# Kernel optimization log

Hardware: AMD Instinct MI355X
Metric: run time of the kernel (lower is better)

Reference implementation:

```python
import jax, jax.numpy as jnp
import numpy as np

N = 4096; TD = 768; ID = 512; H = 256; NH = 4; HD = H // NH; NC = 3; E = 131072


def _gcn(x, w, b, src, dst, n):
    # GCNConv: add self loops, sym-normalize, aggregate at dst
    loop = jnp.arange(n)
    s = jnp.concatenate([src, loop])
    d = jnp.concatenate([dst, loop])
    deg = jax.ops.segment_sum(jnp.ones(s.shape[0], x.dtype), d, num_segments=n)
    dinv = jnp.where(deg > 0, jax.lax.rsqrt(deg), 0.0)
    norm = dinv[s] * dinv[d]                      # [E+N]
    h = x @ w                                     # [N,H] transform
    out = jax.ops.segment_sum(norm[:, None] * h[s], d, num_segments=n)
    return out + b


def setup_inputs() -> dict:
    key = jax.random.key(0)
    ks = jax.random.split(key, 20)
    p = lambda k, shp, sc: jax.random.normal(k, shp, jnp.float32) * sc
    inp = {
        "text_features": jax.random.normal(ks[0], (N, TD), jnp.float32),
        "image_features": jax.random.normal(ks[1], (N, ID), jnp.float32),
        "edge_index": jax.random.randint(ks[2], (2, E), 0, N, jnp.int32),
        "text_w": p(ks[3], (TD, H), 0.02), "text_b": jnp.zeros((H,), jnp.float32),
        "image_w": p(ks[4], (ID, H), 0.02), "image_b": jnp.zeros((H,), jnp.float32),
        "wq": p(ks[5], (H, H), 0.02), "bq": jnp.zeros((H,), jnp.float32),
        "wk": p(ks[6], (H, H), 0.02), "bk": jnp.zeros((H,), jnp.float32),
        "wv": p(ks[7], (H, H), 0.02), "bv": jnp.zeros((H,), jnp.float32),
        "wo": p(ks[8], (H, H), 0.02), "bo": jnp.zeros((H,), jnp.float32),
        "gcn1_w": p(ks[9], (H, H), 0.02), "gcn1_b": jnp.zeros((H,), jnp.float32),
        "gcn2_w": p(ks[10], (H, H), 0.02), "gcn2_b": jnp.zeros((H,), jnp.float32),
        "cls_w": p(ks[11], (H, NC), 0.02), "cls_b": jnp.zeros((NC,), jnp.float32),
    }
    return inp


def reference(text_features, image_features, edge_index,
              text_w, text_b, image_w, image_b,
              wq, bq, wk, bk, wv, bv, wo, bo,
              gcn1_w, gcn1_b, gcn2_w, gcn2_b, cls_w, cls_b):
    # fused linear+relu projections, then elementwise fuse of sum
    combined = (jax.nn.relu(text_features @ text_w + text_b)
                + jax.nn.relu(image_features @ image_w + image_b))  # [N,H]
    # MHA over all nodes (seq_len=N, batch=1)
    q = (combined @ wq + bq).reshape(N, NH, HD)
    k = (combined @ wk + bk).reshape(N, NH, HD)
    v = (combined @ wv + bv).reshape(N, NH, HD)
    scores = jnp.einsum('nhd,mhd->hnm', q, k) / jnp.sqrt(jnp.float32(HD))
    attn = jax.nn.softmax(scores, axis=-1)
    o = jnp.einsum('hnm,mhd->nhd', attn, v).reshape(N, H)
    attn_out = o @ wo + bo
    # two GCN layers
    src, dst = edge_index[0], edge_index[1]
    g1 = jax.nn.relu(_gcn(attn_out, gcn1_w, gcn1_b, src, dst, N))
    g2 = _gcn(g1, gcn2_w, gcn2_b, src, dst, N)
    return g2 @ cls_w + cls_b
```

## Files before the change

kernel.cpp:

```cpp
#include <hip/hip_runtime.h>
#include <hip/hip_bf16.h>

typedef unsigned short ushort;
typedef __attribute__((ext_vector_type(8))) short short8;
typedef __attribute__((ext_vector_type(4))) float f32x4;

constexpr int N_  = 4096;
constexpr int TD_ = 768;
constexpr int ID_ = 512;
constexpr int H_  = 256;
constexpr int HD_ = 64;
constexpr int E_  = 131072;
constexpr int SPLITS = 8;
constexpr float QSCALE = 0.125f * 1.44269504088896f;

#define MFMA16(a, b, c) __builtin_amdgcn_mfma_f32_16x16x32_bf16(a, b, c, 0, 0, 0)

__device__ inline ushort f2bf(float x) {
    union { float f; unsigned u; } v; v.f = x;
    unsigned r = v.u + 0x7fff + ((v.u >> 16) & 1);
    return (ushort)(r >> 16);
}
__device__ inline float lo2f(unsigned u) { union { unsigned x; float f; } v; v.x = u << 16; return v.f; }
__device__ inline float hi2f(unsigned u) { union { unsigned x; float f; } v; v.x = u & 0xffff0000u; return v.f; }

__device__ inline float exp2r(float x) {
    float r;
    asm("v_exp_f32 %0, %1" : "=v"(r) : "v"(x));
    return r;
}
__device__ inline unsigned pkbf(float lo, float hi) {
    union { float f; unsigned u; } a, b; a.f = lo; b.f = hi;
    return __builtin_amdgcn_perm(b.u + 0x8000u, a.u + 0x8000u, 0x07060302u);
}

__device__ inline void gl_lds16(const void* g, void* l) {
    __builtin_amdgcn_global_load_lds((const __attribute__((address_space(1))) unsigned int*)g,
                                     (__attribute__((address_space(3))) unsigned int*)l, 16, 0, 0);
}

__device__ inline void stage64(const ushort* g, long long strideEl, ushort* lds, int w, int l) {
    int r8 = l >> 3;
    int cc = (l & 7) ^ r8;
    #pragma unroll
    for (int p = 0; p < 2; p++) {
        int row = w * 16 + p * 8 + r8;
        gl_lds16(g + (long long)row * strideEl + cc * 8, lds + (w * 16 + p * 8) * 64);
    }
}
__device__ inline void stageB16(const ushort* g, long long strideEl, ushort* lds, int w, int l) {
    if (w < 2) {
        int r8 = l >> 3;
        int row = w * 8 + r8;
        int cc = (l & 7) ^ (row & 7);
        gl_lds16(g + (long long)row * strideEl + cc * 8, lds + w * 512);
    }
}
__device__ inline int swz(int row, int kOff) {
    return row * 64 + ((((kOff >> 3) ^ (row & 7))) << 3);
}


__global__ __launch_bounds__(256) void k_init(int* __restrict__ indeg, int* __restrict__ pos) {
    int i = blockIdx.x * 256 + threadIdx.x;
    indeg[i] = 0;
    pos[i] = 0;
}

__global__ __launch_bounds__(1024) void k_scan(const int* __restrict__ indeg, int* __restrict__ offs,
                                               float* __restrict__ dinv) {
    __shared__ int sums[1024];
    int t = threadIdx.x;
    int b = t * 4;
    int a0 = indeg[b], a1 = indeg[b + 1], a2 = indeg[b + 2], a3 = indeg[b + 3];
    int s = a0 + a1 + a2 + a3;
    sums[t] = s;
    __syncthreads();
    for (int off = 1; off < 1024; off <<= 1) {
        int vv = (t >= off) ? sums[t - off] : 0;
        __syncthreads();
        sums[t] += vv;
        __syncthreads();
    }
    int excl = sums[t] - s;
    offs[b]     = excl;
    offs[b + 1] = excl + a0;
    offs[b + 2] = excl + a0 + a1;
    offs[b + 3] = excl + a0 + a1 + a2;
    dinv[b]     = 1.f / sqrtf((float)(a0 + 1));
    dinv[b + 1] = 1.f / sqrtf((float)(a1 + 1));
    dinv[b + 2] = 1.f / sqrtf((float)(a2 + 1));
    dinv[b + 3] = 1.f / sqrtf((float)(a3 + 1));
}

__global__ __launch_bounds__(256) void k_scatter(const int* __restrict__ src, const int* __restrict__ dst,
                                                 const int* __restrict__ offs, const float* __restrict__ dinv,
                                                 int* __restrict__ pos, int* __restrict__ ssrc,
                                                 float* __restrict__ sw) {
    int e = blockIdx.x * 256 + threadIdx.x;
    int s = src[e], d = dst[e];
    int p = atomicAdd(&pos[d], 1);
    int idx = offs[d] + p;
    ssrc[idx] = s;
    sw[idx] = dinv[s] * dinv[d];
}


__global__ __launch_bounds__(256) void k_prep(const float* __restrict__ text, const float* __restrict__ img,
                                              const float* __restrict__ tw, const float* __restrict__ iw,
                                              const float* __restrict__ wq, const float* __restrict__ wk,
                                              const float* __restrict__ wv, const float* __restrict__ wo,
                                              const float* __restrict__ g1w, const float* __restrict__ g2w,
                                              const int* __restrict__ edst, int* __restrict__ indeg,
                                              ushort* __restrict__ textbf, ushort* __restrict__ imgbf,
                                              ushort* __restrict__ wobf,
                                              ushort* __restrict__ twT, ushort* __restrict__ iwT,
                                              ushort* __restrict__ wqT, ushort* __restrict__ wkT,
                                              ushort* __restrict__ wvT, ushort* __restrict__ g1wT,
                                              ushort* __restrict__ g2wT) {
    __shared__ float Ts[64][65];
    const int b = blockIdx.x;
    const int t = threadIdx.x;
    if (b >= 2752) {
        int e = (b - 2752) * 256 + t;
        atomicAdd(&indeg[edst[e]], 1);
        return;
    }
    if (b < 2592) {
        size_t base = ((size_t)b * 256 + t) * 8;
        const size_t TXE = (size_t)N_ * TD_, IME = (size_t)N_ * ID_;
        const float* src; ushort* dst;
        if (base < TXE) { src = text + base; dst = textbf + base; }
        else if (base < TXE + IME) { src = img + (base - TXE); dst = imgbf + (base - TXE); }
        else { src = wo + (base - TXE - IME); dst = wobf + (base - TXE - IME); }
        float4 x = *(const float4*)src;
        float4 y = *(const float4*)(src + 4);
        ushort o[8] = { f2bf(x.x), f2bf(x.y), f2bf(x.z), f2bf(x.w),
                        f2bf(y.x), f2bf(y.y), f2bf(y.z), f2bf(y.w) };
        *(short8*)dst = *(const short8*)o;
        return;
    }
    int wb = b - 2592;
    const float* src; ushort* dst; int R, tile;
    if (wb < 48)       { src = tw;  dst = twT;  R = 768; tile = wb; }
    else if (wb < 80)  { src = iw;  dst = iwT;  R = 512; tile = wb - 48; }
    else if (wb < 96)  { src = wq;  dst = wqT;  R = 256; tile = wb - 80; }
    else if (wb < 112) { src = wk;  dst = wkT;  R = 256; tile = wb - 96; }
    else if (wb < 128) { src = wv;  dst = wvT;  R = 256; tile = wb - 112; }
    else if (wb < 144) { src = g1w; dst = g1wT; R = 256; tile = wb - 128; }
    else               { src = g2w; dst = g2wT; R = 256; tile = wb - 144; }
    const int r0 = (tile >> 2) * 64, c0 = (tile & 3) * 64;
    #pragma unroll
    for (int u = 0; u < 16; u++) {
        int lin = t + u * 256;
        int r = lin >> 6, c = lin & 63;
        Ts[r][c] = src[(size_t)(r0 + r) * 256 + c0 + c];
    }
    __syncthreads();
    #pragma unroll
    for (int u = 0; u < 16; u++) {
        int lin = t + u * 256;
        int c = lin >> 6, r = lin & 63;
        dst[(size_t)(c0 + c) * R + r0 + r] = f2bf(Ts[r][c]);
    }
}


__global__ __launch_bounds__(256) void k_foldw(const ushort* __restrict__ g1wT, const ushort* __restrict__ wobf,
                                               const float* __restrict__ bo,
                                               ushort* __restrict__ WpT, float* __restrict__ bp) {
    __shared__ ushort As[2][4096];
    __shared__ ushort Bs[2][4096];
    __shared__ ushort Cs[64 * 72];
    const int t = threadIdx.x;
    if (blockIdx.x == 16) {
        float acc = 0.f;
        const ushort* row = g1wT + (size_t)t * 256;
        for (int m8 = 0; m8 < 256; m8 += 8) {
            #pragma unroll
            for (int j = 0; j < 8; j++) acc += bo[m8 + j] * lo2f(((unsigned)row[m8 + j]) << 16);
        }
        bp[t] = acc;
        return;
    }
    const int bm = (blockIdx.x >> 2) * 64, bn = (blockIdx.x & 3) * 64;
    const int w = t >> 6, l = t & 63, q = l >> 4, i = l & 15;
    f32x4 acc[4];
    #pragma unroll
    for (int nt = 0; nt < 4; nt++) acc[nt] = (f32x4){0, 0, 0, 0};
    stage64(g1wT + (size_t)bm * H_, H_, As[0], w, l);
    stage64(wobf + (size_t)bn * H_, H_, Bs[0], w, l);
    for (int c = 0; c < 4; c++) {
        __syncthreads();
        if (c < 3) {
            stage64(g1wT + (size_t)bm * H_ + (c + 1) * 64, H_, As[(c + 1) & 1], w, l);
            stage64(wobf + (size_t)bn * H_ + (c + 1) * 64, H_, Bs[(c + 1) & 1], w, l);
        }
        const ushort* Ab = As[c & 1];
        const ushort* Bb = Bs[c & 1];
        #pragma unroll
        for (int kb = 0; kb < 2; kb++) {
            short8 af = *(const short8*)&Ab[swz(w * 16 + i, kb * 32 + q * 8)];
            #pragma unroll
            for (int nt = 0; nt < 4; nt++) {
                short8 bfr = *(const short8*)&Bb[swz(nt * 16 + i, kb * 32 + q * 8)];
                acc[nt] = MFMA16(af, bfr, acc[nt]);
            }
        }
    }
    __syncthreads();
    #pragma unroll
    for (int nt = 0; nt < 4; nt++)
        #pragma unroll
        for (int r = 0; r < 4; r++)
            Cs[(w * 16 + q * 4 + r) * 72 + nt * 16 + i] = f2bf(acc[nt][r]);
    __syncthreads();
    int rr = t >> 2, c16 = (t & 3) * 16;
    short8 v0 = *(const short8*)&Cs[rr * 72 + c16];
    short8 v1 = *(const short8*)&Cs[rr * 72 + c16 + 8];
    ushort* dst = WpT + (size_t)(bm + rr) * H_ + bn + c16;
    *(short8*)dst = v0;
    *(short8*)(dst + 8) = v1;
}


__global__ __launch_bounds__(256, 4) void k_combined16(const ushort* __restrict__ text, const ushort* __restrict__ img,
                                                       const ushort* __restrict__ twT, const ushort* __restrict__ iwT,
                                                       const float* __restrict__ tb, const float* __restrict__ ib,
                                                       ushort* __restrict__ out) {
    __shared__ ushort As[2][4096];
    __shared__ ushort Bs[2][1024];
    __shared__ ushort Cs[64 * 24];
    const int bm = blockIdx.x * 64, bn = blockIdx.y * 16;
    const int t = threadIdx.x, w = t >> 6, l = t & 63, q = l >> 4, i = l & 15;
    f32x4 acc1 = {0, 0, 0, 0}, acc2 = {0, 0, 0, 0};
    auto stC = [&](int c, int buf) {
        if (c < 12) {
            stage64(text + (size_t)bm * TD_ + c * 64, TD_, As[buf], w, l);
            stageB16(twT + (size_t)bn * TD_ + c * 64, TD_, Bs[buf], w, l);
        } else {
            stage64(img + (size_t)bm * ID_ + (c - 12) * 64, ID_, As[buf], w, l);
            stageB16(iwT + (size_t)bn * ID_ + (c - 12) * 64, ID_, Bs[buf], w, l);
        }
    };
    stC(0, 0);
    for (int c = 0; c < 20; c++) {
        __syncthreads();
        if (c + 1 < 20) stC(c + 1, (c + 1) & 1);
        const ushort* Ab = As[c & 1];
        const ushort* Bb = Bs[c & 1];
        #pragma unroll
        for (int kb = 0; kb < 2; kb++) {
            short8 af = *(const short8*)&Ab[swz(w * 16 + i, kb * 32 + q * 8)];
            short8 bfr = *(const short8*)&Bb[swz(i, kb * 32 + q * 8)];
            if (c < 12) acc1 = MFMA16(af, bfr, acc1);
            else        acc2 = MFMA16(af, bfr, acc2);
        }
    }
    __syncthreads();
    float b1 = tb[bn + i], b2 = ib[bn + i];
    #pragma unroll
    for (int r = 0; r < 4; r++) {
        float v = fmaxf(acc1[r] + b1, 0.f) + fmaxf(acc2[r] + b2, 0.f);
        Cs[(w * 16 + q * 4 + r) * 24 + i] = f2bf(v);
    }
    __syncthreads();
    if (t < 128) {
        int row = t >> 1, h8 = (t & 1) * 8;
        *(short8*)(out + (size_t)(bm + row) * H_ + bn + h8) = *(const short8*)&Cs[row * 24 + h8];
    }
}


__global__ __launch_bounds__(256) void k_qkv_mfma(const ushort* __restrict__ A,
                                                  const ushort* __restrict__ WqT, const ushort* __restrict__ WkT,
                                                  const ushort* __restrict__ WvT,
                                                  const float* __restrict__ bq, const float* __restrict__ bk,
                                                  const float* __restrict__ bv,
                                                  ushort* __restrict__ Qg, ushort* __restrict__ Kg,
                                                  ushort* __restrict__ Vtg) {
    __shared__ ushort As[2][4096];
    __shared__ ushort Bs[2][4096];
    __shared__ ushort Cs[64 * 72];
    const int bm = blockIdx.x * 64, head = blockIdx.y, z = blockIdx.z;
    const ushort* WT = (z == 0) ? WqT : (z == 1) ? WkT : WvT;
    const float* bias = (z == 0) ? bq : (z == 1) ? bk : bv;
    const int t = threadIdx.x, w = t >> 6, l = t & 63, q = l >> 4, i = l & 15;
    f32x4 acc[4];
    #pragma unroll
    for (int nt = 0; nt < 4; nt++) acc[nt] = (f32x4){0,0,0,0};

    stage64(A + (size_t)bm * H_, H_, As[0], w, l);
    stage64(WT + (size_t)(head * 64) * H_, H_, Bs[0], w, l);
    for (int c = 0; c < 4; c++) {
        __syncthreads();
        if (c < 3) {
            stage64(A + (size_t)bm * H_ + (c + 1) * 64, H_, As[(c + 1) & 1], w, l);
            stage64(WT + (size_t)(head * 64) * H_ + (c + 1) * 64, H_, Bs[(c + 1) & 1], w, l);
        }
        const ushort* Ab = As[c & 1];
        const ushort* Bb = Bs[c & 1];
        #pragma unroll
        for (int kb = 0; kb < 2; kb++) {
            short8 af = *(const short8*)&Ab[swz(w * 16 + i, kb * 32 + q * 8)];
            #pragma unroll
            for (int nt = 0; nt < 4; nt++) {
                short8 bfr = *(const short8*)&Bb[swz(nt * 16 + i, kb * 32 + q * 8)];
                acc[nt] = MFMA16(af, bfr, acc[nt]);
            }
        }
    }
    __syncthreads();
    #pragma unroll
    for (int nt = 0; nt < 4; nt++) {
        float bv_ = bias[head * 64 + nt * 16 + i];
        #pragma unroll
        for (int r = 0; r < 4; r++) {
            float v = acc[nt][r] + bv_;
            if (z == 0) v *= QSCALE;
            if (z < 2) Cs[(w * 16 + q * 4 + r) * 72 + nt * 16 + i] = f2bf(v);
            else       Cs[(nt * 16 + i) * 72 + w * 16 + q * 4 + r] = f2bf(v);
        }
    }
    __syncthreads();
    int rr = t >> 2, c16 = (t & 3) * 16;
    short8 v0 = *(const short8*)&Cs[rr * 72 + c16];
    short8 v1 = *(const short8*)&Cs[rr * 72 + c16 + 8];
    ushort* dst;
    if (z < 2) dst = ((z == 0) ? Qg : Kg) + (size_t)head * N_ * HD_ + (size_t)(bm + rr) * HD_ + c16;
    else       dst = Vtg + (size_t)head * HD_ * N_ + (size_t)rr * N_ + bm + c16;
    *(short8*)dst = v0;
    *(short8*)(dst + 8) = v1;
}


__global__ __launch_bounds__(256) void k_attn_mfma(const ushort* __restrict__ Qg, const ushort* __restrict__ Kg,
                                                   const ushort* __restrict__ Vtg, ushort* __restrict__ Op,
                                                   float* __restrict__ lp) {
    __shared__ ushort Ks[4096];
    __shared__ ushort Vs[4096];
    __shared__ ushort Ps[4][16 * 72];
    const int head = blockIdx.y, r0 = blockIdx.x * 64, z = blockIdx.z;
    const int t = threadIdx.x, w = t >> 6, l = t & 63, q = l >> 4, i = l & 15;
    const int rw = (i ^ (i >> 1)) & 7;
    ushort* Pw = &Ps[w][0];

    short8 qf[2];
    #pragma unroll
    for (int kb = 0; kb < 2; kb++)
        qf[kb] = *(const short8*)(Qg + ((size_t)head * N_ + r0 + w * 16 + i) * HD_ + kb * 32 + q * 8);

    f32x4 Oacc[4];
    float lacc = 0.f;
    #pragma unroll
    for (int dt = 0; dt < 4; dt++) Oacc[dt] = (f32x4){0, 0, 0, 0};

    const int NT = 64 / SPLITS;
    const int cb0 = z * NT;
    for (int it = 0; it < NT; it++) {
        const int cb = cb0 + it;
        __syncthreads();
        stage64(Kg + ((size_t)head * N_ + (size_t)cb * 64) * HD_, HD_, Ks, w, l);
        stage64(Vtg + (size_t)head * HD_ * N_ + cb * 64, N_, Vs, w, l);
        __syncthreads();

        f32x4 St[4];
        #pragma unroll
        for (int kt = 0; kt < 4; kt++) St[kt] = (f32x4){0, 0, 0, 0};
        #pragma unroll
        for (int kb = 0; kb < 2; kb++) {
            #pragma unroll
            for (int kt = 0; kt < 4; kt++) {
                short8 kf = *(const short8*)&Ks[swz(kt * 16 + i, kb * 32 + q * 8)];
                St[kt] = MFMA16(kf, qf[kb], St[kt]);
            }
        }
        #pragma unroll
        for (int kt = 0; kt < 4; kt++) {
            float p0 = exp2r(St[kt][0]), p1 = exp2r(St[kt][1]);
            float p2 = exp2r(St[kt][2]), p3 = exp2r(St[kt][3]);
            lacc += (p0 + p1) + (p2 + p3);
            int off = i * 72 + (((2 * kt + (q >> 1)) ^ rw) << 3) + ((q & 1) << 2);
            uint2 v; v.x = pkbf(p0, p1); v.y = pkbf(p2, p3);
            *(uint2*)&Pw[off] = v;
        }
        #pragma unroll
        for (int kb = 0; kb < 2; kb++) {
            short8 pf = *(const short8*)&Pw[i * 72 + (((4 * kb + q) ^ rw) << 3)];
            #pragma unroll
            for (int dt = 0; dt < 4; dt++) {
                short8 vf = *(const short8*)&Vs[swz(dt * 16 + i, kb * 32 + q * 8)];
                Oacc[dt] = MFMA16(vf, pf, Oacc[dt]);
            }
        }
    }

    lacc += __shfl_xor(lacc, 16);
    lacc += __shfl_xor(lacc, 32);

    const size_t sh = ((size_t)z * 4 + head) * N_;
    const int row = r0 + w * 16 + i;
    #pragma unroll
    for (int dt = 0; dt < 4; dt++) {
        uint2 v;
        v.x = pkbf(Oacc[dt][0], Oacc[dt][1]);
        v.y = pkbf(Oacc[dt][2], Oacc[dt][3]);
        *(uint2*)&Op[(sh + row) * HD_ + dt * 16 + q * 4] = v;
    }
    if (l < 16) lp[sh + r0 + w * 16 + l] = lacc;
}

__global__ __launch_bounds__(256) void k_attn_merge(const ushort* __restrict__ Op, const float* __restrict__ lp,
                                                    ushort* __restrict__ obuf) {
    const int t = threadIdx.x;
    const int idx = blockIdx.x * 16 + (t >> 4);
    const int h = idx >> 12, n = idx & 4095;
    const int d4 = (t & 15) * 4;
    float lsum = 0.f;
    float acc[4] = {0.f, 0.f, 0.f, 0.f};
    #pragma unroll
    for (int s = 0; s < SPLITS; s++) {
        size_t sh = ((size_t)s * 4 + h) * N_ + n;
        lsum += lp[sh];
        uint2 o4 = *(const uint2*)&Op[sh * HD_ + d4];
        acc[0] += lo2f(o4.x); acc[1] += hi2f(o4.x);
        acc[2] += lo2f(o4.y); acc[3] += hi2f(o4.y);
    }
    float inv = 1.f / lsum;
    uint2 res;
    res.x = pkbf(acc[0] * inv, acc[1] * inv);
    res.y = pkbf(acc[2] * inv, acc[3] * inv);
    *(uint2*)&obuf[(size_t)n * H_ + h * HD_ + d4] = res;
}


template <bool BIAS>
__global__ __launch_bounds__(256, 4) void k_gemm16(const ushort* __restrict__ A, const ushort* __restrict__ BT,
                                                   const float* __restrict__ bias, ushort* __restrict__ outb) {
    __shared__ ushort As[2][4096];
    __shared__ ushort Bs[2][1024];
    __shared__ ushort Cs[64 * 24];
    const int bm = blockIdx.x * 64, bn = blockIdx.y * 16;
    const int t = threadIdx.x, w = t >> 6, l = t & 63, q = l >> 4, i = l & 15;
    f32x4 acc = {0, 0, 0, 0};
    stage64(A + (size_t)bm * H_, H_, As[0], w, l);
    stageB16(BT + (size_t)bn * H_, H_, Bs[0], w, l);
    for (int c = 0; c < 4; c++) {
        __syncthreads();
        if (c < 3) {
            stage64(A + (size_t)bm * H_ + (c + 1) * 64, H_, As[(c + 1) & 1], w, l);
            stageB16(BT + (size_t)bn * H_ + (c + 1) * 64, H_, Bs[(c + 1) & 1], w, l);
        }
        const ushort* Ab = As[c & 1];
        const ushort* Bb = Bs[c & 1];
        #pragma unroll
        for (int kb = 0; kb < 2; kb++) {
            short8 af = *(const short8*)&Ab[swz(w * 16 + i, kb * 32 + q * 8)];
            short8 bfr = *(const short8*)&Bb[swz(i, kb * 32 + q * 8)];
            acc = MFMA16(af, bfr, acc);
        }
    }
    __syncthreads();
    float bb = BIAS ? bias[bn + i] : 0.f;
    #pragma unroll
    for (int r = 0; r < 4; r++)
        Cs[(w * 16 + q * 4 + r) * 24 + i] = f2bf(acc[r] + bb);
    __syncthreads();
    if (t < 128) {
        int row = t >> 1, h8 = (t & 1) * 8;
        *(short8*)(outb + (size_t)(bm + row) * H_ + bn + h8) = *(const short8*)&Cs[row * 24 + h8];
    }
}


__global__ __launch_bounds__(256) void k_agg1(const ushort* __restrict__ h, const int* __restrict__ ssrc,
                                              const float* __restrict__ sw, const int* __restrict__ offs,
                                              const int* __restrict__ indeg, const float* __restrict__ dinv,
                                              const float* __restrict__ bias, ushort* __restrict__ outb) {
    const int t = threadIdx.x;
    const int j = blockIdx.x * 4 + (t >> 6);
    const int d0 = (t & 63) * 4;
    float dj = dinv[j];
    uint2 hv = *(const uint2*)&h[(size_t)j * H_ + d0];
    float s2 = dj * dj;
    float a0 = s2 * lo2f(hv.x), a1 = s2 * hi2f(hv.x), a2 = s2 * lo2f(hv.y), a3 = s2 * hi2f(hv.y);
    int start = offs[j], cnt = indeg[j];
    for (int e = 0; e < cnt; e++) {
        int s = ssrc[start + e];
        float wg = sw[start + e];
        uint2 v = *(const uint2*)&h[(size_t)s * H_ + d0];
        a0 += wg * lo2f(v.x); a1 += wg * hi2f(v.x);
        a2 += wg * lo2f(v.y); a3 += wg * hi2f(v.y);
    }
    a0 = fmaxf(a0 + bias[d0], 0.f);
    a1 = fmaxf(a1 + bias[d0 + 1], 0.f);
    a2 = fmaxf(a2 + bias[d0 + 2], 0.f);
    a3 = fmaxf(a3 + bias[d0 + 3], 0.f);
    uint2 o;
    o.x = pkbf(a0, a1);
    o.y = pkbf(a2, a3);
    *(uint2*)&outb[(size_t)j * H_ + d0] = o;
}


__global__ __launch_bounds__(256) void k_aggcls(const ushort* __restrict__ h, const int* __restrict__ ssrc,
                                                const float* __restrict__ sw, const int* __restrict__ offs,
                                                const int* __restrict__ indeg, const float* __restrict__ dinv,
                                                const float* __restrict__ bias, const float* __restrict__ cw,
                                                const float* __restrict__ cb, float* __restrict__ out) {
    const int t = threadIdx.x;
    const int j = blockIdx.x * 4 + (t >> 6);
    const int lane = t & 63;
    const int d0 = lane * 4;
    float dj = dinv[j];
    uint2 hv = *(const uint2*)&h[(size_t)j * H_ + d0];
    float s2 = dj * dj;
    float a0 = s2 * lo2f(hv.x), a1 = s2 * hi2f(hv.x), a2 = s2 * lo2f(hv.y), a3 = s2 * hi2f(hv.y);
    int start = offs[j], cnt = indeg[j];
    for (int e = 0; e < cnt; e++) {
        int s = ssrc[start + e];
        float wg = sw[start + e];
        uint2 v = *(const uint2*)&h[(size_t)s * H_ + d0];
        a0 += wg * lo2f(v.x); a1 += wg * hi2f(v.x);
        a2 += wg * lo2f(v.y); a3 += wg * hi2f(v.y);
    }
    a0 += bias[d0]; a1 += bias[d0 + 1]; a2 += bias[d0 + 2]; a3 += bias[d0 + 3];
    float p0 = a0 * cw[d0 * 3 + 0] + a1 * cw[(d0 + 1) * 3 + 0]
             + a2 * cw[(d0 + 2) * 3 + 0] + a3 * cw[(d0 + 3) * 3 + 0];
    float p1 = a0 * cw[d0 * 3 + 1] + a1 * cw[(d0 + 1) * 3 + 1]
             + a2 * cw[(d0 + 2) * 3 + 1] + a3 * cw[(d0 + 3) * 3 + 1];
    float p2 = a0 * cw[d0 * 3 + 2] + a1 * cw[(d0 + 1) * 3 + 2]
             + a2 * cw[(d0 + 2) * 3 + 2] + a3 * cw[(d0 + 3) * 3 + 2];
    #pragma unroll
    for (int off = 32; off > 0; off >>= 1) {
        p0 += __shfl_xor(p0, off);
        p1 += __shfl_xor(p1, off);
        p2 += __shfl_xor(p2, off);
    }
    if (lane == 0) {
        out[j * 3 + 0] = p0 + cb[0];
        out[j * 3 + 1] = p1 + cb[1];
        out[j * 3 + 2] = p2 + cb[2];
    }
}


extern "C" void kernel_launch(void* const* d_in, const int* in_sizes, int n_in,
                              void* d_out, int out_size, void* d_ws, size_t ws_size,
                              hipStream_t stream) {
    const float* text = (const float*)d_in[0];
    const float* img  = (const float*)d_in[1];
    const int*   eidx = (const int*)d_in[2];
    const float* tw  = (const float*)d_in[3];
    const float* tb  = (const float*)d_in[4];
    const float* iw  = (const float*)d_in[5];
    const float* ib  = (const float*)d_in[6];
    const float* wq  = (const float*)d_in[7];
    const float* bq  = (const float*)d_in[8];
    const float* wk  = (const float*)d_in[9];
    const float* bk  = (const float*)d_in[10];
    const float* wv  = (const float*)d_in[11];
    const float* bv  = (const float*)d_in[12];
    const float* wo  = (const float*)d_in[13];
    const float* bo  = (const float*)d_in[14];
    const float* g1w = (const float*)d_in[15];
    const float* g1b = (const float*)d_in[16];
    const float* g2w = (const float*)d_in[17];
    const float* g2b = (const float*)d_in[18];
    const float* cw  = (const float*)d_in[19];
    const float* cbv = (const float*)d_in[20];

    char* W = (char*)d_ws;
    size_t cur = 0;
    auto alloc = [&](size_t sz) { char* p = W + cur; cur += (sz + 255) & ~(size_t)255; return p; };

    float* dinv  = (float*)alloc(N_ * 4);
    float* swv   = (float*)alloc(E_ * 4);
    int* indeg   = (int*)alloc(N_ * 4);
    int* offs    = (int*)alloc(N_ * 4);
    int* pos     = (int*)alloc(N_ * 4);
    int* ssrc    = (int*)alloc(E_ * 4);
    ushort* Qg   = (ushort*)alloc((size_t)N_ * H_ * 2);
    ushort* Kg   = (ushort*)alloc((size_t)N_ * H_ * 2);
    ushort* Vtg  = (ushort*)alloc((size_t)N_ * H_ * 2);
    ushort* obuf = (ushort*)alloc((size_t)N_ * H_ * 2);
    ushort* WpT  = (ushort*)alloc((size_t)H_ * H_ * 2);
    float* bp    = (float*)alloc(H_ * 4);
    ushort* g1wT = (ushort*)alloc((size_t)H_ * H_ * 2);
    ushort* g2wT = (ushort*)alloc((size_t)H_ * H_ * 2);
    ushort* wobf = (ushort*)alloc((size_t)H_ * H_ * 2);
    float* lp    = (float*)alloc((size_t)SPLITS * 4 * N_ * 4);
    char* S = W + cur;

    ushort* textbf = (ushort*)S;
    ushort* imgbf  = textbf + (size_t)N_ * TD_;
    ushort* twT    = imgbf + (size_t)N_ * ID_;
    ushort* iwT    = twT + (size_t)TD_ * H_;
    ushort* wqT    = iwT + (size_t)ID_ * H_;
    ushort* wkT    = wqT + (size_t)H_ * H_;
    ushort* wvT    = wkT + (size_t)H_ * H_;
    ushort* combbf = wvT + (size_t)H_ * H_;
    ushort* Op = (ushort*)S;
    ushort* hbuf  = (ushort*)S;
    ushort* g1b16 = (ushort*)(S + (size_t)2 * 1024 * 1024);
    ushort* hbuf2 = (ushort*)(S + (size_t)4 * 1024 * 1024);

    const int* esrc = eidx;
    const int* edst = eidx + E_;

    k_init<<<dim3(N_ / 256), dim3(256), 0, stream>>>(indeg, pos);
    k_prep<<<dim3(3264), dim3(256), 0, stream>>>(text, img, tw, iw, wq, wk, wv, wo, g1w, g2w,
                                                 edst, indeg,
                                                 textbf, imgbf, wobf, twT, iwT, wqT, wkT, wvT, g1wT, g2wT);
    k_scan<<<dim3(1), dim3(1024), 0, stream>>>(indeg, offs, dinv);
    k_scatter<<<dim3(E_ / 256), dim3(256), 0, stream>>>(esrc, edst, offs, dinv, pos, ssrc, swv);
    k_foldw<<<dim3(17), dim3(256), 0, stream>>>(g1wT, wobf, bo, WpT, bp);

    k_combined16<<<dim3(64, 16), dim3(256), 0, stream>>>(textbf, imgbf, twT, iwT, tb, ib, combbf);
    k_qkv_mfma<<<dim3(64, 4, 3), dim3(256), 0, stream>>>(combbf, wqT, wkT, wvT, bq, bk, bv, Qg, Kg, Vtg);
    k_attn_mfma<<<dim3(64, 4, SPLITS), dim3(256), 0, stream>>>(Qg, Kg, Vtg, Op, lp);
    k_attn_merge<<<dim3(1024), dim3(256), 0, stream>>>(Op, lp, obuf);

    k_gemm16<true><<<dim3(64, 16), dim3(256), 0, stream>>>(obuf, WpT, bp, hbuf);
    k_agg1<<<dim3(N_ / 4), dim3(256), 0, stream>>>(hbuf, ssrc, swv, offs, indeg, dinv, g1b, g1b16);
    k_gemm16<false><<<dim3(64, 16), dim3(256), 0, stream>>>(g1b16, g2wT, nullptr, hbuf2);
    k_aggcls<<<dim3(N_ / 4), dim3(256), 0, stream>>>(hbuf2, ssrc, swv, offs, indeg, dinv, g2b, cw, cbv,
                                                     (float*)d_out);
}
```

Measured before the change: 239.5 us.

## Merge scatter and weight-fold kernels; double-buffer K/V tiles in attention

The edge scatter kernel and the Wo·G1 weight-fold kernel are merged into one launch with block-index dispatch. This removes one kernel launch and lets the two independent jobs run side by side. Separately, the attention kernel now double-buffers its K and V shared-memory tiles, so the next chunk loads while the current one computes, and one barrier per iteration is dropped. The cost is doubled LDS use in attention, which may lower occupancy, and scatter blocks now reserve the fold kernel's shared memory.

```diff
diff --git a/kernel.cpp b/kernel.cpp
--- a/kernel.cpp
+++ b/kernel.cpp
@@ -93,16 +93,76 @@
     dinv[b + 3] = 1.f / sqrtf((float)(a3 + 1));
 }
 
-__global__ __launch_bounds__(256) void k_scatter(const int* __restrict__ src, const int* __restrict__ dst,
-                                                 const int* __restrict__ offs, const float* __restrict__ dinv,
-                                                 int* __restrict__ pos, int* __restrict__ ssrc,
-                                                 float* __restrict__ sw) {
-    int e = blockIdx.x * 256 + threadIdx.x;
-    int s = src[e], d = dst[e];
-    int p = atomicAdd(&pos[d], 1);
-    int idx = offs[d] + p;
-    ssrc[idx] = s;
-    sw[idx] = dinv[s] * dinv[d];
+
+__global__ __launch_bounds__(256) void k_scatfold(const int* __restrict__ src, const int* __restrict__ dst,
+                                                  const int* __restrict__ offs, const float* __restrict__ dinv,
+                                                  int* __restrict__ pos, int* __restrict__ ssrc,
+                                                  float* __restrict__ sw,
+                                                  const ushort* __restrict__ g1wT, const ushort* __restrict__ wobf,
+                                                  const float* __restrict__ bo,
+                                                  ushort* __restrict__ WpT, float* __restrict__ bp) {
+    __shared__ ushort As[2][4096];
+    __shared__ ushort Bs[2][4096];
+    __shared__ ushort Cs[64 * 72];
+    const int t = threadIdx.x;
+    if (blockIdx.x < 512) {
+        int e = blockIdx.x * 256 + t;
+        int s = src[e], d = dst[e];
+        int p = atomicAdd(&pos[d], 1);
+        int idx = offs[d] + p;
+        ssrc[idx] = s;
+        sw[idx] = dinv[s] * dinv[d];
+        return;
+    }
+    if (blockIdx.x == 528) {
+        float acc = 0.f;
+        const ushort* row = g1wT + (size_t)t * 256;
+        for (int m8 = 0; m8 < 256; m8 += 8) {
+            #pragma unroll
+            for (int j = 0; j < 8; j++) acc += bo[m8 + j] * lo2f(((unsigned)row[m8 + j]) << 16);
+        }
+        bp[t] = acc;
+        return;
+    }
+    const int f = blockIdx.x - 512;
+    const int bm = (f >> 2) * 64, bn = (f & 3) * 64;
+    const int w = t >> 6, l = t & 63, q = l >> 4, i = l & 15;
+    f32x4 acc[4];
+    #pragma unroll
+    for (int nt = 0; nt < 4; nt++) acc[nt] = (f32x4){0, 0, 0, 0};
+    stage64(g1wT + (size_t)bm * H_, H_, As[0], w, l);
+    stage64(wobf + (size_t)bn * H_, H_, Bs[0], w, l);
+    for (int c = 0; c < 4; c++) {
+        __syncthreads();
+        if (c < 3) {
+            stage64(g1wT + (size_t)bm * H_ + (c + 1) * 64, H_, As[(c + 1) & 1], w, l);
+            stage64(wobf + (size_t)bn * H_ + (c + 1) * 64, H_, Bs[(c + 1) & 1], w, l);
+        }
+        const ushort* Ab = As[c & 1];
+        const ushort* Bb = Bs[c & 1];
+        #pragma unroll
+        for (int kb = 0; kb < 2; kb++) {
+            short8 af = *(const short8*)&Ab[swz(w * 16 + i, kb * 32 + q * 8)];
+            #pragma unroll
+            for (int nt = 0; nt < 4; nt++) {
+                short8 bfr = *(const short8*)&Bb[swz(nt * 16 + i, kb * 32 + q * 8)];
+                acc[nt] = MFMA16(af, bfr, acc[nt]);
+            }
+        }
+    }
+    __syncthreads();
+    #pragma unroll
+    for (int nt = 0; nt < 4; nt++)
+        #pragma unroll
+        for (int r = 0; r < 4; r++)
+            Cs[(w * 16 + q * 4 + r) * 72 + nt * 16 + i] = f2bf(acc[nt][r]);
+    __syncthreads();
+    int rr = t >> 2, c16 = (t & 3) * 16;
+    short8 v0 = *(const short8*)&Cs[rr * 72 + c16];
+    short8 v1 = *(const short8*)&Cs[rr * 72 + c16 + 8];
+    ushort* dstp = WpT + (size_t)(bm + rr) * H_ + bn + c16;
+    *(short8*)dstp = v0;
+    *(short8*)(dstp + 8) = v1;
 }
 
 
@@ -166,64 +226,6 @@
 }
 
 
-__global__ __launch_bounds__(256) void k_foldw(const ushort* __restrict__ g1wT, const ushort* __restrict__ wobf,
-                                               const float* __restrict__ bo,
-                                               ushort* __restrict__ WpT, float* __restrict__ bp) {
-    __shared__ ushort As[2][4096];
-    __shared__ ushort Bs[2][4096];
-    __shared__ ushort Cs[64 * 72];
-    const int t = threadIdx.x;
-    if (blockIdx.x == 16) {
-        float acc = 0.f;
-        const ushort* row = g1wT + (size_t)t * 256;
-        for (int m8 = 0; m8 < 256; m8 += 8) {
-            #pragma unroll
-            for (int j = 0; j < 8; j++) acc += bo[m8 + j] * lo2f(((unsigned)row[m8 + j]) << 16);
-        }
-        bp[t] = acc;
-        return;
-    }
-    const int bm = (blockIdx.x >> 2) * 64, bn = (blockIdx.x & 3) * 64;
-    const int w = t >> 6, l = t & 63, q = l >> 4, i = l & 15;
-    f32x4 acc[4];
-    #pragma unroll
-    for (int nt = 0; nt < 4; nt++) acc[nt] = (f32x4){0, 0, 0, 0};
-    stage64(g1wT + (size_t)bm * H_, H_, As[0], w, l);
-    stage64(wobf + (size_t)bn * H_, H_, Bs[0], w, l);
-    for (int c = 0; c < 4; c++) {
-        __syncthreads();
-        if (c < 3) {
-            stage64(g1wT + (size_t)bm * H_ + (c + 1) * 64, H_, As[(c + 1) & 1], w, l);
-            stage64(wobf + (size_t)bn * H_ + (c + 1) * 64, H_, Bs[(c + 1) & 1], w, l);
-        }
-        const ushort* Ab = As[c & 1];
-        const ushort* Bb = Bs[c & 1];
-        #pragma unroll
-        for (int kb = 0; kb < 2; kb++) {
-            short8 af = *(const short8*)&Ab[swz(w * 16 + i, kb * 32 + q * 8)];
-            #pragma unroll
-            for (int nt = 0; nt < 4; nt++) {
-                short8 bfr = *(const short8*)&Bb[swz(nt * 16 + i, kb * 32 + q * 8)];
-                acc[nt] = MFMA16(af, bfr, acc[nt]);
-            }
-        }
-    }
-    __syncthreads();
-    #pragma unroll
-    for (int nt = 0; nt < 4; nt++)
-        #pragma unroll
-        for (int r = 0; r < 4; r++)
-            Cs[(w * 16 + q * 4 + r) * 72 + nt * 16 + i] = f2bf(acc[nt][r]);
-    __syncthreads();
-    int rr = t >> 2, c16 = (t & 3) * 16;
-    short8 v0 = *(const short8*)&Cs[rr * 72 + c16];
-    short8 v1 = *(const short8*)&Cs[rr * 72 + c16 + 8];
-    ushort* dst = WpT + (size_t)(bm + rr) * H_ + bn + c16;
-    *(short8*)dst = v0;
-    *(short8*)(dst + 8) = v1;
-}
-
-
 __global__ __launch_bounds__(256, 4) void k_combined16(const ushort* __restrict__ text, const ushort* __restrict__ img,
                                                        const ushort* __restrict__ twT, const ushort* __restrict__ iwT,
                                                        const float* __restrict__ tb, const float* __restrict__ ib,
@@ -337,9 +339,9 @@
 __global__ __launch_bounds__(256) void k_attn_mfma(const ushort* __restrict__ Qg, const ushort* __restrict__ Kg,
                                                    const ushort* __restrict__ Vtg, ushort* __restrict__ Op,
                                                    float* __restrict__ lp) {
-    __shared__ ushort Ks[4096];
-    __shared__ ushort Vs[4096];
-    __shared__ ushort Ps[4][16 * 72];
+    __shared__ ushort Ks[2][4096];
+    __shared__ ushort Vs[2][4096];
+    __shared__ ushort Ps[4][1152];
     const int head = blockIdx.y, r0 = blockIdx.x * 64, z = blockIdx.z;
     const int t = threadIdx.x, w = t >> 6, l = t & 63, q = l >> 4, i = l & 15;
     const int rw = (i ^ (i >> 1)) & 7;
@@ -357,12 +359,17 @@
 
     const int NT = 64 / SPLITS;
     const int cb0 = z * NT;
+    stage64(Kg + ((size_t)head * N_ + (size_t)cb0 * 64) * HD_, HD_, Ks[0], w, l);
+    stage64(Vtg + (size_t)head * HD_ * N_ + cb0 * 64, N_, Vs[0], w, l);
     for (int it = 0; it < NT; it++) {
-        const int cb = cb0 + it;
         __syncthreads();
-        stage64(Kg + ((size_t)head * N_ + (size_t)cb * 64) * HD_, HD_, Ks, w, l);
-        stage64(Vtg + (size_t)head * HD_ * N_ + cb * 64, N_, Vs, w, l);
-        __syncthreads();
+        if (it + 1 < NT) {
+            const int cb = cb0 + it + 1;
+            stage64(Kg + ((size_t)head * N_ + (size_t)cb * 64) * HD_, HD_, Ks[(it + 1) & 1], w, l);
+            stage64(Vtg + (size_t)head * HD_ * N_ + cb * 64, N_, Vs[(it + 1) & 1], w, l);
+        }
+        const ushort* Kb = Ks[it & 1];
+        const ushort* Vb = Vs[it & 1];
 
         f32x4 St[4];
         #pragma unroll
@@ -371,7 +378,7 @@
         for (int kb = 0; kb < 2; kb++) {
             #pragma unroll
             for (int kt = 0; kt < 4; kt++) {
-                short8 kf = *(const short8*)&Ks[swz(kt * 16 + i, kb * 32 + q * 8)];
+                short8 kf = *(const short8*)&Kb[swz(kt * 16 + i, kb * 32 + q * 8)];
                 St[kt] = MFMA16(kf, qf[kb], St[kt]);
             }
         }
@@ -389,7 +396,7 @@
             short8 pf = *(const short8*)&Pw[i * 72 + (((4 * kb + q) ^ rw) << 3)];
             #pragma unroll
             for (int dt = 0; dt < 4; dt++) {
-                short8 vf = *(const short8*)&Vs[swz(dt * 16 + i, kb * 32 + q * 8)];
+                short8 vf = *(const short8*)&Vb[swz(dt * 16 + i, kb * 32 + q * 8)];
                 Oacc[dt] = MFMA16(vf, pf, Oacc[dt]);
             }
         }
@@ -613,8 +620,8 @@
                                                  edst, indeg,
                                                  textbf, imgbf, wobf, twT, iwT, wqT, wkT, wvT, g1wT, g2wT);
     k_scan<<<dim3(1), dim3(1024), 0, stream>>>(indeg, offs, dinv);
-    k_scatter<<<dim3(E_ / 256), dim3(256), 0, stream>>>(esrc, edst, offs, dinv, pos, ssrc, swv);
-    k_foldw<<<dim3(17), dim3(256), 0, stream>>>(g1wT, wobf, bo, WpT, bp);
+    k_scatfold<<<dim3(529), dim3(256), 0, stream>>>(esrc, edst, offs, dinv, pos, ssrc, swv,
+                                                    g1wT, wobf, bo, WpT, bp);
 
     k_combined16<<<dim3(64, 16), dim3(256), 0, stream>>>(textbf, imgbf, twT, iwT, tb, ib, combbf);
     k_qkv_mfma<<<dim3(64, 4, 3), dim3(256), 0, stream>>>(combbf, wqT, wkT, wvT, bq, bk, bv, Qg, Kg, Vtg);
```

Result: no change. 242.5 us (+1.2%).

## Fold graph preprocessing and weight folding into GEMM kernel launches

Applied to the files above, without the earlier changes.

Merges the degree scan into an extra block of the combined-projection kernel, and the edge scatter plus Wo·W1 weight folding into extra blocks of the QKV kernel. This cuts three kernel launches, including a serial single-block scan, and lets the small side tasks overlap with the GEMM blocks. The scan is rewritten for 256 threads with 16 elements each. It also marks the node index as wave-uniform via readfirstlane in the aggregation kernels. The cost is heterogeneous blocks inside one kernel, which may skew scheduling and shared-memory occupancy.

```diff
diff --git a/kernel.cpp b/kernel.cpp
--- a/kernel.cpp
+++ b/kernel.cpp
@@ -65,44 +65,6 @@
     int i = blockIdx.x * 256 + threadIdx.x;
     indeg[i] = 0;
     pos[i] = 0;
-}
-
-__global__ __launch_bounds__(1024) void k_scan(const int* __restrict__ indeg, int* __restrict__ offs,
-                                               float* __restrict__ dinv) {
-    __shared__ int sums[1024];
-    int t = threadIdx.x;
-    int b = t * 4;
-    int a0 = indeg[b], a1 = indeg[b + 1], a2 = indeg[b + 2], a3 = indeg[b + 3];
-    int s = a0 + a1 + a2 + a3;
-    sums[t] = s;
-    __syncthreads();
-    for (int off = 1; off < 1024; off <<= 1) {
-        int vv = (t >= off) ? sums[t - off] : 0;
-        __syncthreads();
-        sums[t] += vv;
-        __syncthreads();
-    }
-    int excl = sums[t] - s;
-    offs[b]     = excl;
-    offs[b + 1] = excl + a0;
-    offs[b + 2] = excl + a0 + a1;
-    offs[b + 3] = excl + a0 + a1 + a2;
-    dinv[b]     = 1.f / sqrtf((float)(a0 + 1));
-    dinv[b + 1] = 1.f / sqrtf((float)(a1 + 1));
-    dinv[b + 2] = 1.f / sqrtf((float)(a2 + 1));
-    dinv[b + 3] = 1.f / sqrtf((float)(a3 + 1));
-}
-
-__global__ __launch_bounds__(256) void k_scatter(const int* __restrict__ src, const int* __restrict__ dst,
-                                                 const int* __restrict__ offs, const float* __restrict__ dinv,
-                                                 int* __restrict__ pos, int* __restrict__ ssrc,
-                                                 float* __restrict__ sw) {
-    int e = blockIdx.x * 256 + threadIdx.x;
-    int s = src[e], d = dst[e];
-    int p = atomicAdd(&pos[d], 1);
-    int idx = offs[d] + p;
-    ssrc[idx] = s;
-    sw[idx] = dinv[s] * dinv[d];
 }
 
 
@@ -166,73 +128,40 @@
 }
 
 
-__global__ __launch_bounds__(256) void k_foldw(const ushort* __restrict__ g1wT, const ushort* __restrict__ wobf,
-                                               const float* __restrict__ bo,
-                                               ushort* __restrict__ WpT, float* __restrict__ bp) {
-    __shared__ ushort As[2][4096];
-    __shared__ ushort Bs[2][4096];
-    __shared__ ushort Cs[64 * 72];
-    const int t = threadIdx.x;
-    if (blockIdx.x == 16) {
-        float acc = 0.f;
-        const ushort* row = g1wT + (size_t)t * 256;
-        for (int m8 = 0; m8 < 256; m8 += 8) {
-            #pragma unroll
-            for (int j = 0; j < 8; j++) acc += bo[m8 + j] * lo2f(((unsigned)row[m8 + j]) << 16);
-        }
-        bp[t] = acc;
-        return;
-    }
-    const int bm = (blockIdx.x >> 2) * 64, bn = (blockIdx.x & 3) * 64;
-    const int w = t >> 6, l = t & 63, q = l >> 4, i = l & 15;
-    f32x4 acc[4];
-    #pragma unroll
-    for (int nt = 0; nt < 4; nt++) acc[nt] = (f32x4){0, 0, 0, 0};
-    stage64(g1wT + (size_t)bm * H_, H_, As[0], w, l);
-    stage64(wobf + (size_t)bn * H_, H_, Bs[0], w, l);
-    for (int c = 0; c < 4; c++) {
-        __syncthreads();
-        if (c < 3) {
-            stage64(g1wT + (size_t)bm * H_ + (c + 1) * 64, H_, As[(c + 1) & 1], w, l);
-            stage64(wobf + (size_t)bn * H_ + (c + 1) * 64, H_, Bs[(c + 1) & 1], w, l);
-        }
-        const ushort* Ab = As[c & 1];
-        const ushort* Bb = Bs[c & 1];
-        #pragma unroll
-        for (int kb = 0; kb < 2; kb++) {
-            short8 af = *(const short8*)&Ab[swz(w * 16 + i, kb * 32 + q * 8)];
-            #pragma unroll
-            for (int nt = 0; nt < 4; nt++) {
-                short8 bfr = *(const short8*)&Bb[swz(nt * 16 + i, kb * 32 + q * 8)];
-                acc[nt] = MFMA16(af, bfr, acc[nt]);
-            }
-        }
-    }
-    __syncthreads();
-    #pragma unroll
-    for (int nt = 0; nt < 4; nt++)
-        #pragma unroll
-        for (int r = 0; r < 4; r++)
-            Cs[(w * 16 + q * 4 + r) * 72 + nt * 16 + i] = f2bf(acc[nt][r]);
-    __syncthreads();
-    int rr = t >> 2, c16 = (t & 3) * 16;
-    short8 v0 = *(const short8*)&Cs[rr * 72 + c16];
-    short8 v1 = *(const short8*)&Cs[rr * 72 + c16 + 8];
-    ushort* dst = WpT + (size_t)(bm + rr) * H_ + bn + c16;
-    *(short8*)dst = v0;
-    *(short8*)(dst + 8) = v1;
-}
-
-
 __global__ __launch_bounds__(256, 4) void k_combined16(const ushort* __restrict__ text, const ushort* __restrict__ img,
                                                        const ushort* __restrict__ twT, const ushort* __restrict__ iwT,
                                                        const float* __restrict__ tb, const float* __restrict__ ib,
-                                                       ushort* __restrict__ out) {
+                                                       const int* __restrict__ indeg, int* __restrict__ offs,
+                                                       float* __restrict__ dinv, ushort* __restrict__ out) {
     __shared__ ushort As[2][4096];
     __shared__ ushort Bs[2][1024];
     __shared__ ushort Cs[64 * 24];
-    const int bm = blockIdx.x * 64, bn = blockIdx.y * 16;
-    const int t = threadIdx.x, w = t >> 6, l = t & 63, q = l >> 4, i = l & 15;
+    __shared__ int sums[256];
+    const int b = blockIdx.x;
+    const int t = threadIdx.x;
+    if (b == 1024) {
+        int v[16]; int ssum = 0; int base = t * 16;
+        #pragma unroll
+        for (int k2 = 0; k2 < 16; k2++) { v[k2] = indeg[base + k2]; ssum += v[k2]; }
+        sums[t] = ssum;
+        __syncthreads();
+        for (int off = 1; off < 256; off <<= 1) {
+            int x = (t >= off) ? sums[t - off] : 0;
+            __syncthreads();
+            sums[t] += x;
+            __syncthreads();
+        }
+        int excl = sums[t] - ssum;
+        #pragma unroll
+        for (int k2 = 0; k2 < 16; k2++) {
+            offs[base + k2] = excl;
+            excl += v[k2];
+            dinv[base + k2] = 1.f / sqrtf((float)(v[k2] + 1));
+        }
+        return;
+    }
+    const int bm = (b >> 4) * 64, bn = (b & 15) * 16;
+    const int w = t >> 6, l = t & 63, q = l >> 4, i = l & 15;
     f32x4 acc1 = {0, 0, 0, 0}, acc2 = {0, 0, 0, 0};
     auto stC = [&](int c, int buf) {
         if (c < 12) {
@@ -272,23 +201,95 @@
 }
 
 
-__global__ __launch_bounds__(256) void k_qkv_mfma(const ushort* __restrict__ A,
-                                                  const ushort* __restrict__ WqT, const ushort* __restrict__ WkT,
-                                                  const ushort* __restrict__ WvT,
-                                                  const float* __restrict__ bq, const float* __restrict__ bk,
-                                                  const float* __restrict__ bv,
-                                                  ushort* __restrict__ Qg, ushort* __restrict__ Kg,
-                                                  ushort* __restrict__ Vtg) {
+__global__ __launch_bounds__(256) void k_qkv_scatfold(const ushort* __restrict__ A,
+                                                      const ushort* __restrict__ WqT, const ushort* __restrict__ WkT,
+                                                      const ushort* __restrict__ WvT,
+                                                      const float* __restrict__ bq, const float* __restrict__ bk,
+                                                      const float* __restrict__ bv,
+                                                      ushort* __restrict__ Qg, ushort* __restrict__ Kg,
+                                                      ushort* __restrict__ Vtg,
+                                                      const int* __restrict__ esrc, const int* __restrict__ edst,
+                                                      const int* __restrict__ offs, const float* __restrict__ dinv,
+                                                      int* __restrict__ pos, int* __restrict__ ssrc,
+                                                      float* __restrict__ swv,
+                                                      const ushort* __restrict__ g1wT, const ushort* __restrict__ wobf,
+                                                      const float* __restrict__ bo,
+                                                      ushort* __restrict__ WpT, float* __restrict__ bp) {
     __shared__ ushort As[2][4096];
     __shared__ ushort Bs[2][4096];
     __shared__ ushort Cs[64 * 72];
-    const int bm = blockIdx.x * 64, head = blockIdx.y, z = blockIdx.z;
+    const int b = blockIdx.x;
+    const int t = threadIdx.x;
+    const int w = t >> 6, l = t & 63, q = l >> 4, i = l & 15;
+
+    if (b >= 768) {
+        if (b < 1280) {
+            int e = (b - 768) * 256 + t;
+            int s = esrc[e], d = edst[e];
+            int p = atomicAdd(&pos[d], 1);
+            int idx = offs[d] + p;
+            ssrc[idx] = s;
+            swv[idx] = dinv[s] * dinv[d];
+            return;
+        }
+        if (b == 1296) {
+            float acc = 0.f;
+            const ushort* row = g1wT + (size_t)t * 256;
+            for (int m8 = 0; m8 < 256; m8 += 8) {
+                #pragma unroll
+                for (int j = 0; j < 8; j++) acc += bo[m8 + j] * lo2f(((unsigned)row[m8 + j]) << 16);
+            }
+            bp[t] = acc;
+            return;
+        }
+        const int f = b - 1280;
+        const int bm = (f >> 2) * 64, bn = (f & 3) * 64;
+        f32x4 acc[4];
+        #pragma unroll
+        for (int nt = 0; nt < 4; nt++) acc[nt] = (f32x4){0, 0, 0, 0};
+        stage64(g1wT + (size_t)bm * H_, H_, As[0], w, l);
+        stage64(wobf + (size_t)bn * H_, H_, Bs[0], w, l);
+        for (int c = 0; c < 4; c++) {
+            __syncthreads();
+            if (c < 3) {
+                stage64(g1wT + (size_t)bm * H_ + (c + 1) * 64, H_, As[(c + 1) & 1], w, l);
+                stage64(wobf + (size_t)bn * H_ + (c + 1) * 64, H_, Bs[(c + 1) & 1], w, l);
+            }
+            const ushort* Ab = As[c & 1];
+            const ushort* Bb = Bs[c & 1];
+            #pragma unroll
+            for (int kb = 0; kb < 2; kb++) {
+                short8 af = *(const short8*)&Ab[swz(w * 16 + i, kb * 32 + q * 8)];
+                #pragma unroll
+                for (int nt = 0; nt < 4; nt++) {
+                    short8 bfr = *(const short8*)&Bb[swz(nt * 16 + i, kb * 32 + q * 8)];
+                    acc[nt] = MFMA16(af, bfr, acc[nt]);
+                }
+            }
+        }
+        __syncthreads();
+        #pragma unroll
+        for (int nt = 0; nt < 4; nt++)
+            #pragma unroll
+            for (int r = 0; r < 4; r++)
+                Cs[(w * 16 + q * 4 + r) * 72 + nt * 16 + i] = f2bf(acc[nt][r]);
+        __syncthreads();
+        int rr = t >> 2, c16 = (t & 3) * 16;
+        short8 v0 = *(const short8*)&Cs[rr * 72 + c16];
+        short8 v1 = *(const short8*)&Cs[rr * 72 + c16 + 8];
+        ushort* dstp = WpT + (size_t)(bm + rr) * H_ + bn + c16;
+        *(short8*)dstp = v0;
+        *(short8*)(dstp + 8) = v1;
+        return;
+    }
+
+    const int z = b >> 8, rem = b & 255;
+    const int bm = (rem >> 2) * 64, head = rem & 3;
     const ushort* WT = (z == 0) ? WqT : (z == 1) ? WkT : WvT;
     const float* bias = (z == 0) ? bq : (z == 1) ? bk : bv;
-    const int t = threadIdx.x, w = t >> 6, l = t & 63, q = l >> 4, i = l & 15;
     f32x4 acc[4];
     #pragma unroll
-    for (int nt = 0; nt < 4; nt++) acc[nt] = (f32x4){0,0,0,0};
+    for (int nt = 0; nt < 4; nt++) acc[nt] = (f32x4){0, 0, 0, 0};
 
     stage64(A + (size_t)bm * H_, H_, As[0], w, l);
     stage64(WT + (size_t)(head * 64) * H_, H_, Bs[0], w, l);
@@ -478,7 +479,7 @@
                                               const int* __restrict__ indeg, const float* __restrict__ dinv,
                                               const float* __restrict__ bias, ushort* __restrict__ outb) {
     const int t = threadIdx.x;
-    const int j = blockIdx.x * 4 + (t >> 6);
+    const int j = __builtin_amdgcn_readfirstlane(blockIdx.x * 4 + (t >> 6));
     const int d0 = (t & 63) * 4;
     float dj = dinv[j];
     uint2 hv = *(const uint2*)&h[(size_t)j * H_ + d0];
@@ -509,7 +510,7 @@
                                                 const float* __restrict__ bias, const float* __restrict__ cw,
                                                 const float* __restrict__ cb, float* __restrict__ out) {
     const int t = threadIdx.x;
-    const int j = blockIdx.x * 4 + (t >> 6);
+    const int j = __builtin_amdgcn_readfirstlane(blockIdx.x * 4 + (t >> 6));
     const int lane = t & 63;
     const int d0 = lane * 4;
     float dj = dinv[j];
@@ -612,12 +613,11 @@
     k_prep<<<dim3(3264), dim3(256), 0, stream>>>(text, img, tw, iw, wq, wk, wv, wo, g1w, g2w,
                                                  edst, indeg,
                                                  textbf, imgbf, wobf, twT, iwT, wqT, wkT, wvT, g1wT, g2wT);
-    k_scan<<<dim3(1), dim3(1024), 0, stream>>>(indeg, offs, dinv);
-    k_scatter<<<dim3(E_ / 256), dim3(256), 0, stream>>>(esrc, edst, offs, dinv, pos, ssrc, swv);
-    k_foldw<<<dim3(17), dim3(256), 0, stream>>>(g1wT, wobf, bo, WpT, bp);
-
-    k_combined16<<<dim3(64, 16), dim3(256), 0, stream>>>(textbf, imgbf, twT, iwT, tb, ib, combbf);
-    k_qkv_mfma<<<dim3(64, 4, 3), dim3(256), 0, stream>>>(combbf, wqT, wkT, wvT, bq, bk, bv, Qg, Kg, Vtg);
+    k_combined16<<<dim3(1025), dim3(256), 0, stream>>>(textbf, imgbf, twT, iwT, tb, ib,
+                                                       indeg, offs, dinv, combbf);
+    k_qkv_scatfold<<<dim3(1297), dim3(256), 0, stream>>>(combbf, wqT, wkT, wvT, bq, bk, bv, Qg, Kg, Vtg,
+                                                         esrc, edst, offs, dinv, pos, ssrc, swv,
+                                                         g1wT, wobf, bo, WpT, bp);
     k_attn_mfma<<<dim3(64, 4, SPLITS), dim3(256), 0, stream>>>(Qg, Kg, Vtg, Op, lp);
     k_attn_merge<<<dim3(1024), dim3(256), 0, stream>>>(Op, lp, obuf);
 
```

Result: faster. 229.1 us (-4.3%).
